# Kernel tuning notes

Measured on AMD Instinct MI355X. Metric: run time of the kernel, lower is better.

The kernel has to match this reference:

```python
import jax, jax.numpy as jnp
import numpy as np

# RPE constants from the source: pix_per_patch=200//16, alpha=12, beta=24, gamma=96, num_buckets=49
ALPHA, BETA, GAMMA, PPP = 12.0, 24.0, 96.0, 12.0
NUM_BUCKETS = 49
LN_EPS = 1e-5


def _layernorm(x, w, b):
    m = jnp.mean(x, axis=-1, keepdims=True)
    v = jnp.mean((x - m) ** 2, axis=-1, keepdims=True)
    return (x - m) / jnp.sqrt(v + LN_EPS) * w + b


def _bucket_ids(ct):
    # ct: (B,T,2) int coords -> piecewise_index bucket ids shifted by beta, (B,T,T) int32
    ctf = ct.astype(jnp.float32)
    diff = ctf[:, :, None, :] - ctf[:, None, :, :]          # (B,T,T,2)
    dist = jnp.sqrt(jnp.sum(diff * diff, axis=-1))           # euclidean distance
    rel = jnp.trunc(dist / PPP)                              # torch.div(..., rounding_mode='trunc')
    abs_r = jnp.abs(rel)
    log_branch = jnp.sign(rel) * jnp.minimum(
        jnp.round(ALPHA + jnp.log(jnp.maximum(abs_r, 1e-6) / ALPHA) / np.log(GAMMA / ALPHA) * (BETA - ALPHA)),
        BETA)
    idx = jnp.where(abs_r <= ALPHA, jnp.round(rel), log_branch).astype(jnp.int32)
    return idx + int(BETA)                                   # shift into [0, num_buckets)


def setup_inputs() -> dict:
    key = jax.random.key(0)
    ks = jax.random.split(key, 12)
    B, T, C, H = 32, 500, 512, 8
    s = 0.02
    return {
        "x": jax.random.normal(ks[0], (B, T, C), jnp.float32),
        "ct": jax.random.randint(ks[1], (B, T, 2), 0, 200, jnp.int32),
        "w_attn": jax.random.normal(ks[2], (C, 3 * C), jnp.float32) * s,
        "b_attn": jnp.zeros((3 * C,), jnp.float32),
        "w_proj": jax.random.normal(ks[3], (C, C), jnp.float32) * s,
        "b_proj": jnp.zeros((C,), jnp.float32),
        "rpe_table": jax.random.normal(ks[4], (H, NUM_BUCKETS), jnp.float32) * s,
        "ln1_w": jnp.ones((C,), jnp.float32),
        "ln1_b": jnp.zeros((C,), jnp.float32),
        "ln2_w": jnp.ones((C,), jnp.float32),
        "ln2_b": jnp.zeros((C,), jnp.float32),
        "w_fc": jax.random.normal(ks[5], (C, 2 * C), jnp.float32) * s,
        "b_fc": jnp.zeros((2 * C,), jnp.float32),
        "w_fc2": jax.random.normal(ks[6], (2 * C, C), jnp.float32) * s,
        "b_fc2": jnp.zeros((C,), jnp.float32),
    }


def reference(x, ct, w_attn, b_attn, w_proj, b_proj, rpe_table,
              ln1_w, ln1_b, ln2_w, ln2_b, w_fc, b_fc, w_fc2, b_fc2):
    B, T, C = x.shape
    H = rpe_table.shape[0]
    D = C // H

    # --- RPEAttention ---
    bucket = _bucket_ids(ct)                                  # (B,T,T) int32 in [0,49)
    qkv = x @ w_attn + b_attn                                 # (B,T,3C)
    q, k, v = jnp.split(qkv, 3, axis=-1)
    q = q.reshape(B, T, H, D).transpose(0, 2, 1, 3)           # (B,H,T,D)
    k = k.reshape(B, T, H, D).transpose(0, 2, 1, 3)
    v = v.reshape(B, T, H, D).transpose(0, 2, 1, 3)
    att = jnp.einsum('bhtd,bhsd->bhts', q, k) * (1.0 / np.sqrt(D))
    # bias buffer is all ones -> masked_fill(bias==0) is a no-op
    # faithful replication of torch: table[:, flat].view(B,H,T,T) (a raw reshape of (H, B*T*T))
    rpe = rpe_table[:, bucket.reshape(-1)].reshape(B, H, T, T)
    att = jax.nn.softmax(att + rpe, axis=-1)
    y = jnp.einsum('bhts,bhsd->bthd', att, v).reshape(B, T, C)
    y = y @ w_proj + b_proj

    # --- Block: residual + LN, MLP (GELU exact), residual + LN ---
    x = _layernorm(x + y, ln1_w, ln1_b)
    h = jax.nn.gelu(x @ w_fc + b_fc, approximate=False)
    x = _layernorm(x + (h @ w_fc2 + b_fc2), ln2_w, ln2_b)
    return x
```

## Files before the change

### kernel.cpp

```cpp
#include <hip/hip_runtime.h>
#include <cstdint>
#include <cstddef>


typedef unsigned short ushort_t;
typedef __bf16 bf16x8 __attribute__((ext_vector_type(8)));
typedef float floatx4 __attribute__((ext_vector_type(4)));
typedef unsigned short ushort4v __attribute__((ext_vector_type(4)));
typedef unsigned short ushort8v __attribute__((ext_vector_type(8)));
typedef unsigned uint2v __attribute__((ext_vector_type(2)));

#define DEV __device__ __forceinline__

#define B_ 32
#define T_ 500
#define C_ 512
#define H_ 8
#define M_ 16000

#define OFF_QK     0ULL
#define OFF_XBF    32800768ULL
#define OFF_BUCKET 49184768ULL
#define OFF_VT     57376768ULL
#define OFF_Y      74153984ULL
#define OFF_WATTN  90537984ULL
#define OFF_WPROJ  92110848ULL
#define OFF_WFC    92635136ULL
#define OFF_WFC2   93683712ULL
#define VT_BYTES   16777216ULL

DEV ushort_t f2bf(float f) {
  union { float f; unsigned u; } v; v.f = f;
  unsigned r = v.u + 0x7fffu + ((v.u >> 16) & 1u);
  return (ushort_t)(r >> 16);
}
DEV float bf2f(ushort_t u) {
  union { unsigned u; float f; } v; v.u = ((unsigned)u) << 16;
  return v.f;
}

DEV void gload16(const void* g, void* l) {
  __builtin_amdgcn_global_load_lds(
      (__attribute__((address_space(1))) void*)(g),
      (__attribute__((address_space(3))) void*)(l), 16, 0, 0);
}

__global__ __launch_bounds__(256) void cvt_bf16(const float* __restrict__ in,
                                                ushort_t* __restrict__ out, int n) {
  int i = (blockIdx.x * 256 + threadIdx.x) * 4;
  if (i >= n) return;
  float4 v = *(const float4*)(in + i);
  ushort4v o = { f2bf(v.x), f2bf(v.y), f2bf(v.z), f2bf(v.w) };
  *(ushort4v*)(out + i) = o;
}

struct WTDesc { const float* w; ushort_t* wt; int K; int N; };
struct WTArgs { WTDesc d[4]; };

__global__ __launch_bounds__(256) void wtrans_all(WTArgs a) {
  const int bid = blockIdx.x;
  int z, local;
  if (bid < 768)       { z = 0; local = bid; }
  else if (bid < 1024) { z = 1; local = bid - 768; }
  else if (bid < 1536) { z = 2; local = bid - 1024; }
  else                 { z = 3; local = bid - 1536; }
  const WTDesc dd = a.d[z];
  const int gx = dd.N >> 5;
  const int n0 = (local % gx) * 32, k0 = (local / gx) * 32;

  __shared__ float tile[32][33];
  const int c = threadIdx.x & 31, r = threadIdx.x >> 5;
#pragma unroll
  for (int rr = 0; rr < 4; ++rr)
    tile[r + rr * 8][c] = dd.w[(size_t)(k0 + r + rr * 8) * dd.N + n0 + c];
  __syncthreads();
#pragma unroll
  for (int rr = 0; rr < 4; ++rr)
    dd.wt[(size_t)(n0 + r + rr * 8) * dd.K + k0 + c] = f2bf(tile[c][r + rr * 8]);
}

__global__ __launch_bounds__(256) void bucket_kernel(const int* __restrict__ ct,
                                                     unsigned char* __restrict__ bucket) {
  const int b = blockIdx.y;
  const int tid = threadIdx.x, w = tid >> 6, lane = tid & 63;
  __shared__ int2 ctS[500];
  for (int j = tid; j < T_; j += 256) ctS[j] = ((const int2*)ct)[(size_t)b * T_ + j];
  __syncthreads();
  const int t = blockIdx.x * 4 + w;
  const int2 a = ctS[t];
  const float ax = (float)a.x, ay = (float)a.y;
  const size_t rowbase = (size_t)(b * T_ + t) << 9;
#pragma unroll
  for (int it = 0; it < 8; ++it) {
    const int s = it * 64 + lane;
    if (s < T_) {
      const int2 c2 = ctS[s];
      const float dx = ax - (float)c2.x, dy = ay - (float)c2.y;
      const float dist = __builtin_amdgcn_sqrtf(dx * dx + dy * dy);
      const float rel = truncf(dist * (1.0f / 12.0f));
      const float far = fminf(
          rintf(fmaf(__builtin_amdgcn_logf(rel * (1.0f / 12.0f)), 4.0f, 12.0f)), 24.0f);
      const float idx = (rel <= 12.0f) ? rel : far;
      bucket[rowbase + (s >> 6) * 64 + (s & 15) * 4 + ((s >> 4) & 3)]
          = (unsigned char)(((int)idx + 24) << 2);
    }
  }
}

__global__ __launch_bounds__(256, 2)
void gemm_qkv(const ushort_t* __restrict__ A,
              const ushort_t* __restrict__ Bt,
              const float* __restrict__ bias,
              ushort_t* __restrict__ qk,
              ushort_t* __restrict__ vt) {
  constexpr int K = 512;
  const int bid = blockIdx.x;
  const int xcd = bid & 7, k = bid >> 3;
  const int n_blk = k % 12, mg = k / 12;
  const int m_blk = mg * 8 + xcd;
  if (m_blk >= 125) return;
  const int m0 = m_blk * 128, n0 = n_blk * 128;

  __shared__ __align__(16) ushort_t As[128 * 64];
  __shared__ __align__(16) ushort_t Bs[128 * 64];
  const int tid = threadIdx.x;
  const int lane = tid & 63, w = tid >> 6;
  const int wm = w >> 1, wn = w & 1;
  const int quad = lane >> 4, l15 = lane & 15;

  floatx4 acc[4][4] = {};

  for (int k0 = 0; k0 < K; k0 += 64) {
    __syncthreads();
#pragma unroll
    for (int j = 0; j < 4; ++j) {
      const int chunk = j * 256 + tid;
      const int row = chunk >> 3, pos = chunk & 7, c = pos ^ (row & 7);
      gload16(A + (size_t)(m0 + row) * K + k0 + c * 8, (char*)As + j * 4096 + w * 1024);
      gload16(Bt + (size_t)(n0 + row) * K + k0 + c * 8, (char*)Bs + j * 4096 + w * 1024);
    }
    asm volatile("s_waitcnt vmcnt(0)" ::: "memory");
    __syncthreads();

#pragma unroll
    for (int kq = 0; kq < 2; ++kq) {
      bf16x8 af[4], bfr[4];
#pragma unroll
      for (int t = 0; t < 4; ++t) {
        const int rowa = wm * 64 + t * 16 + l15;
        const int posa = (kq * 4 + quad) ^ (rowa & 7);
        af[t] = *(const bf16x8*)((const char*)As + rowa * 128 + posa * 16);
        const int rowb = wn * 64 + t * 16 + l15;
        const int posb = (kq * 4 + quad) ^ (rowb & 7);
        bfr[t] = *(const bf16x8*)((const char*)Bs + rowb * 128 + posb * 16);
      }
#pragma unroll
      for (int tm = 0; tm < 4; ++tm)
#pragma unroll
        for (int tn = 0; tn < 4; ++tn)
          acc[tm][tn] = __builtin_amdgcn_mfma_f32_16x16x32_bf16(af[tm], bfr[tn], acc[tm][tn], 0, 0, 0);
    }
  }

  if (n0 < 1024) {
    const float qs = (n0 < 512) ? 0.18033688f : 1.0f;
#pragma unroll
    for (int tn = 0; tn < 4; ++tn) {
      const int n = n0 + wn * 64 + tn * 16 + l15;
      const float bs = bias[n];
#pragma unroll
      for (int tm = 0; tm < 4; ++tm)
#pragma unroll
        for (int r = 0; r < 4; ++r) {
          const int m = m0 + wm * 64 + tm * 16 + quad * 4 + r;
          qk[(size_t)m * 1024 + n] = f2bf((acc[tm][tn][r] + bs) * qs);
        }
    }
  } else {
#pragma unroll
    for (int tn = 0; tn < 4; ++tn) {
      const int n = n0 + wn * 64 + tn * 16 + l15;
      const float bs = bias[n];
      const int hh = (n >> 6) - 16, dd = n & 63;
#pragma unroll
      for (int tm = 0; tm < 4; ++tm) {
        const int mb = m0 + wm * 64 + tm * 16 + quad * 4;
        const int bb = mb / 500;
        const int ss = mb - bb * 500;
        ushort4v pk;
#pragma unroll
        for (int r = 0; r < 4; ++r) pk[r] = f2bf(acc[tm][tn][r] + bs);
        *(ushort4v*)(vt + (((size_t)(bb * 8 + hh)) * 64 + dd) * 512 + ss) = pk;
      }
    }
  }
}

template <int TN, int EPI>
__global__ __launch_bounds__(256, TN == 64 ? 4 : 2)
void gemm_bt(const ushort_t* __restrict__ A,
             const ushort_t* __restrict__ Bt,
             const float* __restrict__ bias,
             const float* __restrict__ resf,
             const ushort_t* __restrict__ resb,
             void* __restrict__ outp,
             int N, int K) {
  constexpr int TMW = (TN == 128) ? 4 : 2;
  const int nn = N / TN;
  const int bid = blockIdx.x;
  const int xcd = bid & 7, kk = bid >> 3;
  const int n_blk = kk % nn, mg = kk / nn;
  const int m_blk = mg * 8 + xcd;
  if (m_blk >= 125) return;
  const int m0 = m_blk * 128, n0 = n_blk * TN;

  __shared__ __align__(16) ushort_t As[128 * 64];
  __shared__ __align__(16) ushort_t Bs[TN * 64];
  const int tid = threadIdx.x;
  const int lane = tid & 63, w = tid >> 6;
  const int wm = (TN == 128) ? (w >> 1) : w;
  const int wn = (TN == 128) ? (w & 1) : 0;
  const int quad = lane >> 4, l15 = lane & 15;

  floatx4 acc[TMW][4] = {};

  for (int k0 = 0; k0 < K; k0 += 64) {
    __syncthreads();
#pragma unroll
    for (int j = 0; j < 4; ++j) {
      const int chunk = j * 256 + tid;
      const int row = chunk >> 3, pos = chunk & 7, c = pos ^ (row & 7);
      gload16(A + (size_t)(m0 + row) * K + k0 + c * 8, (char*)As + j * 4096 + w * 1024);
    }
#pragma unroll
    for (int j = 0; j < TN / 32; ++j) {
      const int chunk = j * 256 + tid;
      const int row = chunk >> 3, pos = chunk & 7, c = pos ^ (row & 7);
      gload16(Bt + (size_t)(n0 + row) * K + k0 + c * 8, (char*)Bs + j * 4096 + w * 1024);
    }
    asm volatile("s_waitcnt vmcnt(0)" ::: "memory");
    __syncthreads();

#pragma unroll
    for (int kq = 0; kq < 2; ++kq) {
      bf16x8 af[TMW], bfr[4];
#pragma unroll
      for (int t = 0; t < TMW; ++t) {
        const int row = wm * (TMW * 16) + t * 16 + l15;
        const int pos = (kq * 4 + quad) ^ (row & 7);
        af[t] = *(const bf16x8*)((const char*)As + row * 128 + pos * 16);
      }
#pragma unroll
      for (int t = 0; t < 4; ++t) {
        const int row = wn * 64 + t * 16 + l15;
        const int pos = (kq * 4 + quad) ^ (row & 7);
        bfr[t] = *(const bf16x8*)((const char*)Bs + row * 128 + pos * 16);
      }
#pragma unroll
      for (int tm = 0; tm < TMW; ++tm)
#pragma unroll
        for (int tn = 0; tn < 4; ++tn)
          acc[tm][tn] = __builtin_amdgcn_mfma_f32_16x16x32_bf16(af[tm], bfr[tn], acc[tm][tn], 0, 0, 0);
    }
  }

#pragma unroll
  for (int tn = 0; tn < 4; ++tn) {
    const int n = n0 + wn * 64 + tn * 16 + l15;
    const float bs = bias[n];
#pragma unroll
    for (int tm = 0; tm < TMW; ++tm) {
#pragma unroll
      for (int r = 0; r < 4; ++r) {
        const int m = m0 + wm * (TMW * 16) + tm * 16 + quad * 4 + r;
        const float v = acc[tm][tn][r] + bs;
        if (EPI == 1) {
          const float gv = 0.5f * v * (1.0f + erff(v * 0.70710678118654752f));
          ((ushort_t*)outp)[(size_t)m * N + n] = f2bf(gv);
        } else if (EPI == 2) {
          ((float*)outp)[(size_t)m * N + n] = v + resf[(size_t)m * N + n];
        } else {
          ((float*)outp)[(size_t)m * N + n] = v + bf2f(resb[(size_t)m * N + n]);
        }
      }
    }
  }
}

DEV floatx4 mfma16(bf16x8 a, bf16x8 b, floatx4 c) {
  return __builtin_amdgcn_mfma_f32_16x16x32_bf16(a, b, c, 0, 0, 0);
}

template <bool LAST>
DEV void qk_softmax(const ushort_t* __restrict__ Ksb, char* pw,
                    const unsigned (&bu)[2][4], const bf16x8 (&qf)[2][2],
                    float (&lsum)[2], const float* __restrict__ gtab,
                    int quad, int l15) {
  floatx4 sc[2][4];
  __builtin_amdgcn_s_setprio(1);
#pragma unroll
  for (int tn = 0; tn < 4; ++tn) {
    const int row = tn * 16 + l15;
    bf16x8 kf[2];
#pragma unroll
    for (int kq = 0; kq < 2; ++kq) {
      const int pos = (kq * 4 + quad) ^ (row & 7);
      kf[kq] = *(const bf16x8*)((const char*)Ksb + row * 128 + pos * 16);
    }
#pragma unroll
    for (int qs = 0; qs < 2; ++qs) {
      floatx4 z = {0.0f, 0.0f, 0.0f, 0.0f};
      z = mfma16(kf[0], qf[qs][0], z);
      z = mfma16(kf[1], qf[qs][1], z);
      sc[qs][tn] = z;
    }
  }
  __builtin_amdgcn_s_setprio(0);

#pragma unroll
  for (int qs = 0; qs < 2; ++qs) {
    const int qrow = qs * 16 + l15;
    char* prow = pw + qrow * 128;
    const int rx = l15 & 7;
#pragma unroll
    for (int tn = 0; tn < 4; ++tn) {
      float tv[4];
#pragma unroll
      for (int r = 0; r < 4; ++r)
        tv[r] = *(const float*)((const char*)gtab + ((bu[qs][r] >> (tn * 8)) & 255u));
      unsigned pk[2];
#pragma unroll
      for (int rp = 0; rp < 2; ++rp) {
        float pp[2];
#pragma unroll
        for (int h2 = 0; h2 < 2; ++h2) {
          const int r = rp * 2 + h2;
          float p = __builtin_amdgcn_exp2f(fmaf(tv[r], 1.44269504f, sc[qs][tn][r]));
          if (LAST && (tn * 16 + quad * 4 + r >= 52)) p = 0.0f;
          lsum[qs] += p;
          pp[h2] = p;
        }
        pk[rp] = __builtin_amdgcn_perm(
            __builtin_bit_cast(unsigned, pp[1]),
            __builtin_bit_cast(unsigned, pp[0]), 0x07060302u);
      }
      uint2v wv; wv[0] = pk[0]; wv[1] = pk[1];
      *(uint2v*)(prow + (((tn * 2 + (quad >> 1)) ^ rx) << 4) + (quad & 1) * 8) = wv;
    }
  }
}

DEV void pv_acc(const ushort_t* __restrict__ Vsb, const char* pw,
                floatx4 (&o)[2][4], int quad, int l15) {
  __builtin_amdgcn_s_setprio(1);
#pragma unroll
  for (int ks = 0; ks < 2; ++ks) {
    bf16x8 vf[4];
#pragma unroll
    for (int nd = 0; nd < 4; ++nd) {
      const int row = nd * 16 + l15;
      const int pos = (ks * 4 + quad) ^ (row & 7);
      vf[nd] = *(const bf16x8*)((const char*)Vsb + row * 128 + pos * 16);
    }
#pragma unroll
    for (int qs = 0; qs < 2; ++qs) {
      const int qrow = qs * 16 + l15;
      const int ppos = (ks * 4 + quad) ^ (l15 & 7);
      const bf16x8 pfr = *(const bf16x8*)(pw + qrow * 128 + ppos * 16);
#pragma unroll
      for (int nd = 0; nd < 4; ++nd)
        o[qs][nd] = mfma16(pfr, vf[nd], o[qs][nd]);
    }
  }
  __builtin_amdgcn_s_setprio(0);
}

__global__ __launch_bounds__(256, 3) void attn_kernel(const ushort_t* __restrict__ qk,
                                                      const ushort_t* __restrict__ vt,
                                                      const unsigned char* __restrict__ bucket,
                                                      const float* __restrict__ rpe,
                                                      ushort_t* __restrict__ y) {
  const int bid = blockIdx.x;
  const int xcd = bid & 7, sl = bid >> 3;
  const int qt = sl & 3;
  const int pair = xcd * 32 + (sl >> 2);
  const int h = pair >> 5, b = pair & 31;
  const int g = b >> 2;
  const int bpp = 8 * (b & 3) + h;

  __shared__ __align__(16) ushort_t Qs[128 * 64];
  __shared__ __align__(16) ushort_t Ks[2][64 * 64];
  __shared__ __align__(16) ushort_t Vs[64 * 64];

  const int tid = threadIdx.x;
  const int lane = tid & 63, w = tid >> 6;
  const int quad = lane >> 4, l15 = lane & 15;
  const int t0 = qt * 128;

#pragma unroll
  for (int j = 0; j < 4; ++j) {
    const int chunk = j * 256 + tid;
    const int row = chunk >> 3, pos = chunk & 7, c = pos ^ (row & 7);
    gload16(qk + (size_t)(b * T_ + t0 + row) * 1024 + h * 64 + c * 8,
            (char*)Qs + j * 4096 + w * 1024);
  }
#pragma unroll
  for (int j = 0; j < 2; ++j) {
    const int chunk = j * 256 + tid;
    const int row = chunk >> 3, pos = chunk & 7, c = pos ^ (row & 7);
    gload16(qk + (size_t)(b * T_ + row) * 1024 + 512 + h * 64 + c * 8,
            (char*)Ks[0] + j * 4096 + w * 1024);
  }

  const float* gtab = rpe + g * 49;

  const unsigned char* bkb[2];
#pragma unroll
  for (int qs = 0; qs < 2; ++qs) {
    const int tr = t0 + w * 32 + qs * 16 + l15;
    const int trc = (tr < T_) ? tr : (T_ - 1);
    bkb[qs] = bucket + ((size_t)(bpp * T_ + trc) << 9) + quad * 16;
  }
  unsigned bu[2][4];
  {
    const uint4 b0 = *(const uint4*)(bkb[0]);
    const uint4 b1 = *(const uint4*)(bkb[1]);
    bu[0][0] = b0.x; bu[0][1] = b0.y; bu[0][2] = b0.z; bu[0][3] = b0.w;
    bu[1][0] = b1.x; bu[1][1] = b1.y; bu[1][2] = b1.z; bu[1][3] = b1.w;
  }

  asm volatile("s_waitcnt vmcnt(0)" ::: "memory");
  __syncthreads();

  bf16x8 qf[2][2];
#pragma unroll
  for (int qs = 0; qs < 2; ++qs)
#pragma unroll
    for (int kq = 0; kq < 2; ++kq) {
      const int row = w * 32 + qs * 16 + l15;
      const int pos = (kq * 4 + quad) ^ (row & 7);
      qf[qs][kq] = *(const bf16x8*)((const char*)Qs + row * 128 + pos * 16);
    }

  floatx4 o[2][4] = {};
  float lsum[2] = {0.0f, 0.0f};
  char* pw = (char*)Qs + w * 4096;

#pragma unroll 1
  for (int st = 0; st < 7; ++st) {
    const int cb = st & 1;
    __syncthreads();
#pragma unroll
    for (int j = 0; j < 2; ++j) {
      const int chunk = j * 256 + tid;
      const int row = chunk >> 3, pos = chunk & 7, c = pos ^ (row & 7);
      gload16(vt + ((size_t)(b * 8 + h) * 64 + row) * 512 + st * 64 + c * 8,
              (char*)Vs + j * 4096 + w * 1024);
      gload16(qk + (size_t)(b * T_ + (st + 1) * 64 + row) * 1024 + 512 + h * 64 + c * 8,
              (char*)Ks[cb ^ 1] + j * 4096 + w * 1024);
    }
    const uint4 b0 = *(const uint4*)(bkb[0] + (st + 1) * 64);
    const uint4 b1 = *(const uint4*)(bkb[1] + (st + 1) * 64);

    qk_softmax<false>(Ks[cb], pw, bu, qf, lsum, gtab, quad, l15);

    asm volatile("s_waitcnt vmcnt(0)" ::: "memory");
    __syncthreads();

    pv_acc(Vs, pw, o, quad, l15);

    bu[0][0] = b0.x; bu[0][1] = b0.y; bu[0][2] = b0.z; bu[0][3] = b0.w;
    bu[1][0] = b1.x; bu[1][1] = b1.y; bu[1][2] = b1.z; bu[1][3] = b1.w;
  }
  __syncthreads();
#pragma unroll
  for (int j = 0; j < 2; ++j) {
    const int chunk = j * 256 + tid;
    const int row = chunk >> 3, pos = chunk & 7, c = pos ^ (row & 7);
    gload16(vt + ((size_t)(b * 8 + h) * 64 + row) * 512 + 448 + c * 8,
            (char*)Vs + j * 4096 + w * 1024);
  }
  qk_softmax<true>(Ks[1], pw, bu, qf, lsum, gtab, quad, l15);
  asm volatile("s_waitcnt vmcnt(0)" ::: "memory");
  __syncthreads();
  pv_acc(Vs, pw, o, quad, l15);

  float lr[2];
#pragma unroll
  for (int qs = 0; qs < 2; ++qs) {
    float s = lsum[qs];
    s += __shfl_xor(s, 16);
    s += __shfl_xor(s, 32);
    lr[qs] = s;
  }
#pragma unroll
  for (int qs = 0; qs < 2; ++qs)
#pragma unroll
    for (int r = 0; r < 4; ++r) {
      const float sv = __shfl(lr[qs], quad * 4 + r);
      const int t = t0 + w * 32 + qs * 16 + quad * 4 + r;
      if (t < T_) {
        const float inv = 1.0f / sv;
#pragma unroll
        for (int nd = 0; nd < 4; ++nd)
          y[((size_t)b * T_ + t) * 512 + h * 64 + nd * 16 + l15] =
              f2bf(o[qs][nd][r] * inv);
      }
    }
}

__global__ __launch_bounds__(256) void ln_kernel(const float* z,
                                                 const float* __restrict__ gw,
                                                 const float* __restrict__ gb,
                                                 ushort_t* out_bf, float* out_f) {
  const int tid = threadIdx.x, lane = tid & 63, w = tid >> 6;
  const int row = blockIdx.x * 4 + w;
  const float* zr = z + (size_t)row * 512;
  const int c0 = lane * 8;
  const float4 v0 = *(const float4*)(zr + c0);
  const float4 v1 = *(const float4*)(zr + c0 + 4);
  float s = ((v0.x + v0.y) + (v0.z + v0.w)) + ((v1.x + v1.y) + (v1.z + v1.w));
#pragma unroll
  for (int m = 1; m < 64; m <<= 1) s += __shfl_xor(s, m);
  const float mean = s * (1.0f / 512.0f);
  float d[8] = { v0.x - mean, v0.y - mean, v0.z - mean, v0.w - mean,
                 v1.x - mean, v1.y - mean, v1.z - mean, v1.w - mean };
  float q = 0.0f;
#pragma unroll
  for (int j = 0; j < 8; ++j) q += d[j] * d[j];
#pragma unroll
  for (int m = 1; m < 64; m <<= 1) q += __shfl_xor(q, m);
  const float rstd = rsqrtf(q * (1.0f / 512.0f) + 1e-5f);
  const float4 ga = *(const float4*)(gw + c0);
  const float4 gc = *(const float4*)(gw + c0 + 4);
  const float4 ba = *(const float4*)(gb + c0);
  const float4 bc = *(const float4*)(gb + c0 + 4);
  float ov[8];
  ov[0] = d[0] * rstd * ga.x + ba.x;
  ov[1] = d[1] * rstd * ga.y + ba.y;
  ov[2] = d[2] * rstd * ga.z + ba.z;
  ov[3] = d[3] * rstd * ga.w + ba.w;
  ov[4] = d[4] * rstd * gc.x + bc.x;
  ov[5] = d[5] * rstd * gc.y + bc.y;
  ov[6] = d[6] * rstd * gc.z + bc.z;
  ov[7] = d[7] * rstd * gc.w + bc.w;
  if (out_bf) {
    ushort8v pk;
#pragma unroll
    for (int j = 0; j < 8; ++j) pk[j] = f2bf(ov[j]);
    *(ushort8v*)(out_bf + (size_t)row * 512 + c0) = pk;
  }
  if (out_f) {
    float4 o0 = { ov[0], ov[1], ov[2], ov[3] };
    float4 o1 = { ov[4], ov[5], ov[6], ov[7] };
    *(float4*)(out_f + (size_t)row * 512 + c0) = o0;
    *(float4*)(out_f + (size_t)row * 512 + c0 + 4) = o1;
  }
}

extern "C" void kernel_launch(void* const* d_in, const int* in_sizes, int n_in,
                              void* d_out, int out_size, void* d_ws, size_t ws_size,
                              hipStream_t stream) {
  (void)in_sizes; (void)n_in; (void)out_size; (void)ws_size;
  const float* x      = (const float*)d_in[0];
  const int*   ct     = (const int*)d_in[1];
  const float* w_attn = (const float*)d_in[2];
  const float* b_attn = (const float*)d_in[3];
  const float* w_proj = (const float*)d_in[4];
  const float* b_proj = (const float*)d_in[5];
  const float* rpe    = (const float*)d_in[6];
  const float* ln1w   = (const float*)d_in[7];
  const float* ln1b   = (const float*)d_in[8];
  const float* ln2w   = (const float*)d_in[9];
  const float* ln2b   = (const float*)d_in[10];
  const float* w_fc   = (const float*)d_in[11];
  const float* b_fc   = (const float*)d_in[12];
  const float* w_fc2  = (const float*)d_in[13];
  const float* b_fc2  = (const float*)d_in[14];
  float* out = (float*)d_out;

  char* ws = (char*)d_ws;
  ushort_t* qk      = (ushort_t*)(ws + OFF_QK);
  ushort_t* h_buf   = (ushort_t*)(ws + OFF_QK);
  ushort_t* x_bf    = (ushort_t*)(ws + OFF_XBF);
  ushort_t* x1      = (ushort_t*)(ws + OFF_XBF);
  unsigned char* bk = (unsigned char*)(ws + OFF_BUCKET);
  ushort_t* vt      = (ushort_t*)(ws + OFF_VT);
  ushort_t* y       = (ushort_t*)(ws + OFF_Y);
  ushort_t* wt_attn = (ushort_t*)(ws + OFF_WATTN);
  ushort_t* wt_proj = (ushort_t*)(ws + OFF_WPROJ);
  ushort_t* wt_fc   = (ushort_t*)(ws + OFF_WFC);
  ushort_t* wt_fc2  = (ushort_t*)(ws + OFF_WFC2);

  cvt_bf16<<<dim3(8000), 256, 0, stream>>>(x, x_bf, M_ * C_);
  WTArgs wta;
  wta.d[0] = { w_attn, wt_attn, 512, 1536 };
  wta.d[1] = { w_proj, wt_proj, 512, 512 };
  wta.d[2] = { w_fc,   wt_fc,   512, 1024 };
  wta.d[3] = { w_fc2,  wt_fc2,  1024, 512 };
  wtrans_all<<<dim3(2048), 256, 0, stream>>>(wta);
  bucket_kernel<<<dim3(125, 32), 256, 0, stream>>>(ct, bk);
  hipMemsetAsync(vt, 0, VT_BYTES, stream);

  gemm_qkv<<<dim3(1536), 256, 0, stream>>>(x_bf, wt_attn, b_attn, qk, vt);
  attn_kernel<<<dim3(1024), 256, 0, stream>>>(qk, vt, bk, rpe, y);
  gemm_bt<64, 2><<<dim3(1024), 256, 0, stream>>>(y, wt_proj, b_proj, x, nullptr, out, 512, 512);
  ln_kernel<<<dim3(4000), 256, 0, stream>>>(out, ln1w, ln1b, x1, nullptr);
  gemm_bt<128, 1><<<dim3(1024), 256, 0, stream>>>(x1, wt_fc, b_fc, nullptr, nullptr, h_buf, 1024, 512);
  gemm_bt<64, 3><<<dim3(1024), 256, 0, stream>>>(h_buf, wt_fc2, b_fc2, nullptr, x1, out, 512, 1024);
  ln_kernel<<<dim3(4000), 256, 0, stream>>>(out, ln2w, ln2b, nullptr, out);
}
```

Baseline: 300.1 us.

## Double-buffer V tiles, fuse QK-softmax with PV, and serve RPE lookups via bpermute

```diff
diff --git a/kernel.cpp b/kernel.cpp
--- a/kernel.cpp
+++ b/kernel.cpp
@@ -292,10 +292,11 @@
 }
 
 template <bool LAST>
-DEV void qk_softmax(const ushort_t* __restrict__ Ksb, char* pw,
-                    const unsigned (&bu)[2][4], const bf16x8 (&qf)[2][2],
-                    float (&lsum)[2], const float* __restrict__ gtab,
-                    int quad, int l15) {
+DEV void attn_tile(const ushort_t* __restrict__ Ksb,
+                   const ushort_t* __restrict__ Vsb, char* pw,
+                   const unsigned (&bu)[2][4], const bf16x8 (&qf)[2][2],
+                   floatx4 (&o)[2][4], float (&lsum)[2],
+                   float treg, int quad, int l15) {
   floatx4 sc[2][4];
   __builtin_amdgcn_s_setprio(1);
 #pragma unroll
@@ -324,10 +325,6 @@
     const int rx = l15 & 7;
 #pragma unroll
     for (int tn = 0; tn < 4; ++tn) {
-      float tv[4];
-#pragma unroll
-      for (int r = 0; r < 4; ++r)
-        tv[r] = *(const float*)((const char*)gtab + ((bu[qs][r] >> (tn * 8)) & 255u));
       unsigned pk[2];
 #pragma unroll
       for (int rp = 0; rp < 2; ++rp) {
@@ -335,7 +332,10 @@
 #pragma unroll
         for (int h2 = 0; h2 < 2; ++h2) {
           const int r = rp * 2 + h2;
-          float p = __builtin_amdgcn_exp2f(fmaf(tv[r], 1.44269504f, sc[qs][tn][r]));
+          const int idx4 = (int)((bu[qs][r] >> (tn * 8)) & 255u);
+          const float tv = __builtin_bit_cast(float,
+              __builtin_amdgcn_ds_bpermute(idx4, __builtin_bit_cast(int, treg)));
+          float p = __builtin_amdgcn_exp2f(sc[qs][tn][r] + tv);
           if (LAST && (tn * 16 + quad * 4 + r >= 52)) p = 0.0f;
           lsum[qs] += p;
           pp[h2] = p;
@@ -348,10 +348,8 @@
       *(uint2v*)(prow + (((tn * 2 + (quad >> 1)) ^ rx) << 4) + (quad & 1) * 8) = wv;
     }
   }
-}
-
-DEV void pv_acc(const ushort_t* __restrict__ Vsb, const char* pw,
-                floatx4 (&o)[2][4], int quad, int l15) {
+  asm volatile("" ::: "memory");
+
   __builtin_amdgcn_s_setprio(1);
 #pragma unroll
   for (int ks = 0; ks < 2; ++ks) {
@@ -390,7 +388,7 @@
 
   __shared__ __align__(16) ushort_t Qs[128 * 64];
   __shared__ __align__(16) ushort_t Ks[2][64 * 64];
-  __shared__ __align__(16) ushort_t Vs[64 * 64];
+  __shared__ __align__(16) ushort_t Vs[2][64 * 64];
 
   const int tid = threadIdx.x;
   const int lane = tid & 63, w = tid >> 6;
@@ -410,9 +408,11 @@
     const int row = chunk >> 3, pos = chunk & 7, c = pos ^ (row & 7);
     gload16(qk + (size_t)(b * T_ + row) * 1024 + 512 + h * 64 + c * 8,
             (char*)Ks[0] + j * 4096 + w * 1024);
-  }
-
-  const float* gtab = rpe + g * 49;
+    gload16(vt + ((size_t)(b * 8 + h) * 64 + row) * 512 + c * 8,
+            (char*)Vs[0] + j * 4096 + w * 1024);
+  }
+
+  const float treg = rpe[g * 49 + (lane < 49 ? lane : 48)] * 1.44269504f;
 
   const unsigned char* bkb[2];
 #pragma unroll
@@ -449,41 +449,27 @@
 #pragma unroll 1
   for (int st = 0; st < 7; ++st) {
     const int cb = st & 1;
-    __syncthreads();
+    const uint4 b0 = *(const uint4*)(bkb[0] + (st + 1) * 64);
+    const uint4 b1 = *(const uint4*)(bkb[1] + (st + 1) * 64);
 #pragma unroll
     for (int j = 0; j < 2; ++j) {
       const int chunk = j * 256 + tid;
       const int row = chunk >> 3, pos = chunk & 7, c = pos ^ (row & 7);
-      gload16(vt + ((size_t)(b * 8 + h) * 64 + row) * 512 + st * 64 + c * 8,
-              (char*)Vs + j * 4096 + w * 1024);
+      gload16(vt + ((size_t)(b * 8 + h) * 64 + row) * 512 + (st + 1) * 64 + c * 8,
+              (char*)Vs[cb ^ 1] + j * 4096 + w * 1024);
       gload16(qk + (size_t)(b * T_ + (st + 1) * 64 + row) * 1024 + 512 + h * 64 + c * 8,
               (char*)Ks[cb ^ 1] + j * 4096 + w * 1024);
     }
-    const uint4 b0 = *(const uint4*)(bkb[0] + (st + 1) * 64);
-    const uint4 b1 = *(const uint4*)(bkb[1] + (st + 1) * 64);
-
-    qk_softmax<false>(Ks[cb], pw, bu, qf, lsum, gtab, quad, l15);
+
+    attn_tile<false>(Ks[cb], Vs[cb], pw, bu, qf, o, lsum, treg, quad, l15);
 
     asm volatile("s_waitcnt vmcnt(0)" ::: "memory");
     __syncthreads();
 
-    pv_acc(Vs, pw, o, quad, l15);
-
     bu[0][0] = b0.x; bu[0][1] = b0.y; bu[0][2] = b0.z; bu[0][3] = b0.w;
     bu[1][0] = b1.x; bu[1][1] = b1.y; bu[1][2] = b1.z; bu[1][3] = b1.w;
   }
-  __syncthreads();
-#pragma unroll
-  for (int j = 0; j < 2; ++j) {
-    const int chunk = j * 256 + tid;
-    const int row = chunk >> 3, pos = chunk & 7, c = pos ^ (row & 7);
-    gload16(vt + ((size_t)(b * 8 + h) * 64 + row) * 512 + 448 + c * 8,
-            (char*)Vs + j * 4096 + w * 1024);
-  }
-  qk_softmax<true>(Ks[1], pw, bu, qf, lsum, gtab, quad, l15);
-  asm volatile("s_waitcnt vmcnt(0)" ::: "memory");
-  __syncthreads();
-  pv_acc(Vs, pw, o, quad, l15);
+  attn_tile<true>(Ks[1], Vs[1], pw, bu, qf, o, lsum, treg, quad, l15);
 
   float lr[2];
 #pragma unroll
```

Result: faster. 291.9 us (-2.8%).
